# Kernel tuning notes

Hardware: AMD Instinct MI355X
Metric: run time of the kernel (lower is better)

The kernel has to match this reference:

```python
import jax, jax.numpy as jnp
import numpy as np

B, S = 32, 2048
NUM_SKILL = 4096
D = 64   # dim_s
M = 32   # size_m


def setup_inputs() -> dict:
    key = jax.random.key(0)
    ks = jax.random.split(key, 16)
    he = (2.0 / D) ** 0.5  # kaiming-normal-ish scale
    return {
        "question": jax.random.randint(ks[0], (B, S), 0, NUM_SKILL),
        "response": jax.random.randint(ks[1], (B, S), 0, 2),
        "skill": jax.random.randint(ks[2], (B, S), 0, NUM_SKILL),
        "mask": jnp.ones((B, S), jnp.float32),
        "k_c_emb": jax.random.normal(ks[3], (NUM_SKILL, D), jnp.float32) * 0.05,
        "v_c_emb": jax.random.normal(ks[4], (2 * NUM_SKILL, D), jnp.float32) * 0.05,
        "Mk": jax.random.normal(ks[5], (M, D), jnp.float32) * he,
        "Mv0": jax.random.normal(ks[6], (M, D), jnp.float32) * he,
        "e_W": jax.random.normal(ks[7], (D, D), jnp.float32) * he,
        "e_b": jnp.zeros((D,), jnp.float32),
        "a_W": jax.random.normal(ks[8], (D, D), jnp.float32) * he,
        "a_b": jnp.zeros((D,), jnp.float32),
        "f_W": jax.random.normal(ks[9], (2 * D, D), jnp.float32) * (2.0 / (2 * D)) ** 0.5,
        "f_b": jnp.zeros((D,), jnp.float32),
        "p_W": jax.random.normal(ks[10], (D, 1), jnp.float32) * he,
        "p_b": jnp.zeros((1,), jnp.float32),
    }


def reference(question, response, skill, mask, k_c_emb, v_c_emb, Mk, Mv0,
              e_W, e_b, a_W, a_b, f_W, f_b, p_W, p_b):
    num_skill = k_c_emb.shape[0]
    batch = question.shape[0]

    xc = skill + num_skill * response          # [B,S]
    k = k_c_emb[skill]                         # [B,S,D]
    v = v_c_emb[xc]                            # [B,S,D]

    w = jax.nn.softmax(jnp.einsum('bsd,md->bsm', k, Mk), axis=-1)  # [B,S,M]
    e = jax.nn.sigmoid(v @ e_W + e_b)          # [B,S,D]
    a = jnp.tanh(v @ a_W + a_b)                # [B,S,D]

    def step(Mvt, inp):
        wt, et, at, mt = inp                   # [B,M],[B,D],[B,D],[B]
        Mvt_next = Mvt * (1.0 - wt[:, :, None] * et[:, None, :]) \
                   + wt[:, :, None] * at[:, None, :]
        Mvt = jnp.where(mt[:, None, None] == 1, Mvt_next, Mvt)
        return Mvt, Mvt

    xs = (jnp.swapaxes(w, 0, 1), jnp.swapaxes(e, 0, 1),
          jnp.swapaxes(a, 0, 1), jnp.swapaxes(mask, 0, 1))
    Mv_init = jnp.broadcast_to(Mv0[None], (batch, M, D))
    _, Mv_states = jax.lax.scan(step, Mv_init, xs)   # [S,B,M,D]; Mv_states[t] = Mv after t+1 updates

    # Mv[:,1:-1] in torch = states after 1..S-1 updates = Mv_states[0:S-1]
    Mv_used = jnp.swapaxes(Mv_states[:-1], 0, 1)      # [B,S-1,M,D]
    read = jnp.einsum('bsm,bsmd->bsd', w[:, 1:], Mv_used)  # [B,S-1,D]
    f = jnp.tanh(jnp.concatenate([read, k[:, 1:]], axis=-1) @ f_W + f_b)
    # dropout is identity in eval mode
    p = (f @ p_W + p_b).squeeze(-1)                   # [B,S-1]
    return p
```

## Files before the change

kernel.cpp:

```cpp
#include <hip/hip_runtime.h>
#include <hip/hip_bf16.h>
#include <math.h>

#define BB 32
#define SS 2048
#define DD 64
#define MM 32
#define NSKILL 4096
#define CC 64
#define LL 32
#define NOUT (BB * (SS - 1))

__device__ __forceinline__ float sigmoidf_(float x) {
    return 1.f / (1.f + __expf(-x));
}
__device__ __forceinline__ float tanhf_(float x) {
    float t = __expf(-2.f * fabsf(x));
    float r = (1.f - t) / (1.f + t);
    return copysignf(r, x);
}

__global__ __launch_bounds__(256, 2) void k_w(
    const int* __restrict__ skill, const float* __restrict__ k_emb,
    const float* __restrict__ Mk, float* __restrict__ w_out)
{
    __shared__ float kst[64][64];
    const int tid = threadIdx.x;
    const int g = blockIdx.x;
    #pragma unroll
    for (int p = 0; p < 4; ++p) {
        const int r = p * 16 + (tid >> 4);
        const int t = g * 64 + r;
        const float4 kv = ((const float4*)(k_emb + (size_t)skill[t] * DD))[tid & 15];
        *(float4*)&kst[r][(tid & 15) * 4] = kv;
    }
    const int l  = tid & 63;
    const int m  = l & 31;
    const int th = l >> 5;
    const int w  = tid >> 6;
    float4 mk4[16];
    const float4* mkp = (const float4*)(Mk + m * DD);
    #pragma unroll
    for (int q = 0; q < 16; ++q) mk4[q] = mkp[q];
    __syncthreads();

    for (int j = 0; j < 8; ++j) {
        const int tl = w * 16 + j * 2 + th;
        const float4* kp = (const float4*)&kst[tl][0];
        float a0 = 0.f, a1 = 0.f, a2 = 0.f, a3 = 0.f;
        #pragma unroll
        for (int q = 0; q < 16; ++q) {
            const float4 kv = kp[q];
            a0 = fmaf(kv.x, mk4[q].x, a0);
            a1 = fmaf(kv.y, mk4[q].y, a1);
            a2 = fmaf(kv.z, mk4[q].z, a2);
            a3 = fmaf(kv.w, mk4[q].w, a3);
        }
        const float lg = (a0 + a1) + (a2 + a3);
        float mx = lg;
        #pragma unroll
        for (int off = 16; off >= 1; off >>= 1) mx = fmaxf(mx, __shfl_xor(mx, off));
        const float ev = __expf(lg - mx);
        float sm = ev;
        #pragma unroll
        for (int off = 16; off >= 1; off >>= 1) sm += __shfl_xor(sm, off);
        w_out[(size_t)(g * 64 + tl) * MM + m] = ev / sm;
    }
}

__global__ __launch_bounds__(256, 2) void k_ea(
    const int* __restrict__ skill, const int* __restrict__ resp,
    const float* __restrict__ v_emb,
    const float* __restrict__ eW, const float* __restrict__ eb,
    const float* __restrict__ aW, const float* __restrict__ ab,
    float* __restrict__ e_out, float* __restrict__ a_out)
{
    __shared__ float vst[64][64];
    const int tid = threadIdx.x;
    const int g = blockIdx.x;
    #pragma unroll
    for (int p = 0; p < 4; ++p) {
        const int r = p * 16 + (tid >> 4);
        const int t = g * 64 + r;
        const int xc = skill[t] + NSKILL * resp[t];
        const float4 vv = ((const float4*)(v_emb + (size_t)xc * DD))[tid & 15];
        *(float4*)&vst[r][(tid & 15) * 4] = vv;
    }
    const int l = tid & 63;
    const int w = tid >> 6;
    float ew[64], aw[64];
    #pragma unroll
    for (int i = 0; i < 64; ++i) ew[i] = eW[i * DD + l];
    #pragma unroll
    for (int i = 0; i < 64; ++i) aw[i] = aW[i * DD + l];
    const float ebd = eb[l], abd = ab[l];
    __syncthreads();

    for (int j = 0; j < 16; ++j) {
        const int tl = w * 16 + j;
        const float4* vp = (const float4*)&vst[tl][0];
        float e0 = ebd, e1 = 0.f, e2 = 0.f, e3 = 0.f;
        float x0 = abd, x1 = 0.f, x2 = 0.f, x3 = 0.f;
        #pragma unroll
        for (int q = 0; q < 16; ++q) {
            const float4 vv = vp[q];
            e0 = fmaf(vv.x, ew[4*q+0], e0);
            e1 = fmaf(vv.y, ew[4*q+1], e1);
            e2 = fmaf(vv.z, ew[4*q+2], e2);
            e3 = fmaf(vv.w, ew[4*q+3], e3);
            x0 = fmaf(vv.x, aw[4*q+0], x0);
            x1 = fmaf(vv.y, aw[4*q+1], x1);
            x2 = fmaf(vv.z, aw[4*q+2], x2);
            x3 = fmaf(vv.w, aw[4*q+3], x3);
        }
        const size_t t = (size_t)(g * 64 + tl);
        e_out[t * DD + l] = sigmoidf_((e0 + e1) + (e2 + e3));
        a_out[t * DD + l] = tanhf_((x0 + x1) + (x2 + x3));
    }
}

__global__ __launch_bounds__(64, 4) void k_pass1(
    const float* __restrict__ w, const float* __restrict__ mask,
    const float* __restrict__ e, const float* __restrict__ a,
    float* __restrict__ Abar, float* __restrict__ Bbar)
{
    __shared__ float4 wl[LL * 16 / 4];
    const int lane = threadIdx.x;
    const int bc = blockIdx.x >> 1;
    const int mh = blockIdx.x & 1;
    const int b = bc / CC;
    const int c = bc % CC;
    const int t0 = c * LL;

    const float4* wg = (const float4*)(w + (size_t)(b * SS + t0) * MM);
    #pragma unroll
    for (int u = 0; u < 2; ++u) {
        const int q4 = u * 64 + lane;
        const int j = q4 >> 2;
        const int q = q4 & 3;
        const float s = (mask[b * SS + t0 + j] == 1.f) ? 1.f : 0.f;
        float4 wq = wg[j * 8 + mh * 4 + q];
        wq.x *= s; wq.y *= s; wq.z *= s; wq.w *= s;
        wl[q4] = wq;
    }
    __syncthreads();

    float Ab[16], Bb[16];
    #pragma unroll
    for (int i = 0; i < 16; ++i) { Ab[i] = 1.f; Bb[i] = 0.f; }

    const float* ep = e + (size_t)(b * SS + t0) * DD + lane;
    const float* ap = a + (size_t)(b * SS + t0) * DD + lane;
    for (int j = 0; j < LL; ++j) {
        const float ed = ep[j * DD];
        const float ad = ap[j * DD];
        const float4* wlj = wl + j * 4;
        #pragma unroll
        for (int u = 0; u < 4; ++u) {
            const float4 wq = wlj[u];
            float t1;
            t1 = fmaf(-wq.x, ed, 1.f); Ab[4*u+0] *= t1; Bb[4*u+0] = fmaf(Bb[4*u+0], t1, wq.x * ad);
            t1 = fmaf(-wq.y, ed, 1.f); Ab[4*u+1] *= t1; Bb[4*u+1] = fmaf(Bb[4*u+1], t1, wq.y * ad);
            t1 = fmaf(-wq.z, ed, 1.f); Ab[4*u+2] *= t1; Bb[4*u+2] = fmaf(Bb[4*u+2], t1, wq.z * ad);
            t1 = fmaf(-wq.w, ed, 1.f); Ab[4*u+3] *= t1; Bb[4*u+3] = fmaf(Bb[4*u+3], t1, wq.w * ad);
        }
    }
    float* Ao = Abar + (size_t)bc * MM * DD + (size_t)(mh * 16) * DD + lane;
    float* Bo = Bbar + (size_t)bc * MM * DD + (size_t)(mh * 16) * DD + lane;
    #pragma unroll
    for (int i = 0; i < 16; ++i) { Ao[i * DD] = Ab[i]; Bo[i * DD] = Bb[i]; }
}

__global__ __launch_bounds__(256, 2) void k_pass2(
    const float* __restrict__ Abar, float* __restrict__ Bbar_cst,
    const float* __restrict__ Mv0)
{
    const int idx = blockIdx.x * 256 + threadIdx.x;
    const int b = idx >> 11;
    const int md = idx & 2047;
    float s = Mv0[md];
    for (int c = 0; c < CC; ++c) {
        const int off = ((b * CC + c) << 11) + md;
        const float sa = Abar[off];
        const float sb = Bbar_cst[off];
        Bbar_cst[off] = s;
        s = fmaf(s, sa, sb);
    }
}

__global__ __launch_bounds__(64, 4) void k_pass3(
    const float* __restrict__ w, const float* __restrict__ mask,
    const float* __restrict__ e, const float* __restrict__ a,
    const float* __restrict__ cstate, float* __restrict__ readv)
{
    __shared__ float4 wl[LL * MM / 4];
    __shared__ float4 wn[LL * MM / 4];
    const int lane = threadIdx.x;
    const int bc = blockIdx.x >> 1;
    const int dh = blockIdx.x & 1;
    const int b = bc / CC;
    const int c = bc % CC;
    const int t0 = c * LL;
    const bool last = (c == CC - 1);
    const int dof = lane & 31;
    const int mh  = lane >> 5;

    const float4* wg  = (const float4*)(w + (size_t)(b * SS + t0) * MM);
    const float4* wg2 = (const float4*)(w + (size_t)(b * SS + t0 + 1) * MM);
    #pragma unroll
    for (int u = 0; u < 4; ++u) {
        const int q4 = u * 64 + lane;
        const int j = q4 >> 3;
        const float s = (mask[b * SS + t0 + j] == 1.f) ? 1.f : 0.f;
        float4 wq = wg[q4];
        wq.x *= s; wq.y *= s; wq.z *= s; wq.w *= s;
        wl[q4] = wq;
        float4 wq2;
        if (last && q4 >= 248) wq2 = make_float4(0.f, 0.f, 0.f, 0.f);
        else                   wq2 = wg2[q4];
        wn[q4] = wq2;
    }
    __syncthreads();

    float Mv[16];
    const float* cs = cstate + (size_t)bc * MM * DD + (size_t)(mh * 16) * DD
                      + dh * 32 + dof;
    #pragma unroll
    for (int i = 0; i < 16; ++i) Mv[i] = cs[i * DD];

    const float* ep = e + (size_t)(b * SS + t0) * DD + dh * 32 + dof;
    const float* ap = a + (size_t)(b * SS + t0) * DD + dh * 32 + dof;
    float* ro = readv + (size_t)(b * SS + t0 + 1) * DD + dh * 32 + dof;
    for (int j = 0; j < LL; ++j) {
        const float ed = ep[j * DD];
        const float ad = ap[j * DD];
        const float4* wlj = wl + j * 8 + mh * 4;
        const float4* wnj = wn + j * 8 + mh * 4;
        float r0 = 0.f, r1 = 0.f, r2 = 0.f, r3 = 0.f;
        #pragma unroll
        for (int u = 0; u < 4; ++u) {
            const float4 wq = wlj[u];
            const float4 w2 = wnj[u];
            float t1;
            t1 = fmaf(-wq.x, ed, 1.f); Mv[4*u+0] = fmaf(Mv[4*u+0], t1, wq.x * ad); r0 = fmaf(w2.x, Mv[4*u+0], r0);
            t1 = fmaf(-wq.y, ed, 1.f); Mv[4*u+1] = fmaf(Mv[4*u+1], t1, wq.y * ad); r1 = fmaf(w2.y, Mv[4*u+1], r1);
            t1 = fmaf(-wq.z, ed, 1.f); Mv[4*u+2] = fmaf(Mv[4*u+2], t1, wq.z * ad); r2 = fmaf(w2.z, Mv[4*u+2], r2);
            t1 = fmaf(-wq.w, ed, 1.f); Mv[4*u+3] = fmaf(Mv[4*u+3], t1, wq.w * ad); r3 = fmaf(w2.w, Mv[4*u+3], r3);
        }
        float r = (r0 + r1) + (r2 + r3);
        r += __shfl_xor(r, 32);
        if (mh == 0 && !(last && j == LL - 1))
            ro[j * DD] = r;
    }
}

__global__ __launch_bounds__(256, 2) void k_final(
    const float* __restrict__ readv, const int* __restrict__ skill,
    const float* __restrict__ k_emb,
    const float* __restrict__ fW, const float* __restrict__ fb,
    const float* __restrict__ pW, const float* __restrict__ pb,
    float* __restrict__ out)
{
    __shared__ float rst[64][64];
    __shared__ float kst[64][64];
    __shared__ float pbuf[64];
    const int tid = threadIdx.x;
    const int g = blockIdx.x;
    #pragma unroll
    for (int p = 0; p < 4; ++p) {
        const int r = p * 16 + (tid >> 4);
        int o = g * 64 + r;
        if (o >= NOUT) o = 0;
        const int b = o / (SS - 1);
        const int s = o - b * (SS - 1) + 1;
        const size_t tok = (size_t)b * SS + s;
        const int q = tid & 15;
        *(float4*)&rst[r][q * 4] = ((const float4*)(readv + tok * DD))[q];
        *(float4*)&kst[r][q * 4] = ((const float4*)(k_emb + (size_t)skill[tok] * DD))[q];
    }
    const int l = tid & 63;
    const int w = tid >> 6;
    float fw[128];
    #pragma unroll
    for (int i = 0; i < 128; ++i) fw[i] = fW[i * DD + l];
    const float fbd = fb[l], pwd = pW[l];
    __syncthreads();

    for (int j = 0; j < 16; ++j) {
        const int tl = w * 16 + j;
        const float4* rp = (const float4*)&rst[tl][0];
        const float4* kp = (const float4*)&kst[tl][0];
        float f0 = fbd, f1 = 0.f, f2 = 0.f, f3 = 0.f;
        #pragma unroll
        for (int q = 0; q < 16; ++q) {
            const float4 rv = rp[q];
            f0 = fmaf(rv.x, fw[4*q+0], f0);
            f1 = fmaf(rv.y, fw[4*q+1], f1);
            f2 = fmaf(rv.z, fw[4*q+2], f2);
            f3 = fmaf(rv.w, fw[4*q+3], f3);
        }
        #pragma unroll
        for (int q = 0; q < 16; ++q) {
            const float4 kv = kp[q];
            f0 = fmaf(kv.x, fw[64+4*q+0], f0);
            f1 = fmaf(kv.y, fw[64+4*q+1], f1);
            f2 = fmaf(kv.z, fw[64+4*q+2], f2);
            f3 = fmaf(kv.w, fw[64+4*q+3], f3);
        }
        float pv = tanhf_((f0 + f1) + (f2 + f3)) * pwd;
        #pragma unroll
        for (int off = 32; off >= 1; off >>= 1) pv += __shfl_xor(pv, off);
        if (l == 0) pbuf[tl] = pv;
    }
    __syncthreads();
    if (tid < 64) {
        const int o = g * 64 + tid;
        if (o < NOUT) out[o] = pbuf[tid] + pb[0];
    }
}

extern "C" void kernel_launch(void* const* d_in, const int* in_sizes, int n_in,
                              void* d_out, int out_size, void* d_ws, size_t ws_size,
                              hipStream_t stream)
{
    const int*   response = (const int*)d_in[1];
    const int*   skill    = (const int*)d_in[2];
    const float* mask     = (const float*)d_in[3];
    const float* k_emb    = (const float*)d_in[4];
    const float* v_emb    = (const float*)d_in[5];
    const float* Mk       = (const float*)d_in[6];
    const float* Mv0      = (const float*)d_in[7];
    const float* eW       = (const float*)d_in[8];
    const float* ebias    = (const float*)d_in[9];
    const float* aW       = (const float*)d_in[10];
    const float* abias    = (const float*)d_in[11];
    const float* fW       = (const float*)d_in[12];
    const float* fbias    = (const float*)d_in[13];
    const float* pW       = (const float*)d_in[14];
    const float* pbias    = (const float*)d_in[15];
    float* out = (float*)d_out;

    float* ws    = (float*)d_ws;
    float* w_    = ws;
    float* e_    = w_    + (size_t)BB * SS * MM;
    float* a_    = e_    + (size_t)BB * SS * DD;
    float* Abar  = a_    + (size_t)BB * SS * DD;
    float* Bbar  = Abar  + (size_t)BB * CC * MM * DD;
    float* readv = Bbar  + (size_t)BB * CC * MM * DD;

    k_w    <<<1024, 256, 0, stream>>>(skill, k_emb, Mk, w_);
    k_ea   <<<1024, 256, 0, stream>>>(skill, response, v_emb,
                                      eW, ebias, aW, abias, e_, a_);
    k_pass1<<<BB * CC * 2, 64, 0, stream>>>(w_, mask, e_, a_, Abar, Bbar);
    k_pass2<<<256,  256, 0, stream>>>(Abar, Bbar, Mv0);
    k_pass3<<<BB * CC * 2, 64, 0, stream>>>(w_, mask, e_, a_, Bbar, readv);
    k_final<<<1024, 256, 0, stream>>>(readv, skill, k_emb, fW, fbias,
                                      pW, pbias, out);
}
```

Before: 216.1 us.

## Fuse w, e/a projection and chunk-scan pass1 into one front kernel

Merges the softmax-weight kernel, the erase/add projection kernel and the first chunked-scan pass into a single kernel. Each block keeps its 64 timesteps of w, e and a in LDS and computes the per-chunk affine composition directly, so pass1 no longer re-reads those tensors from global memory. Two waves split each 32-step chunk and combine their results through LDS. The pass2 carry loop is also unrolled by four so its loads are issued together. The cost is much higher LDS use per block (about 58 KB), which may limit occupancy, and a less parallel pass1 phase inside the fused kernel.

```diff
diff --git a/kernel.cpp b/kernel.cpp
--- a/kernel.cpp
+++ b/kernel.cpp
@@ -20,144 +20,137 @@
     return copysignf(r, x);
 }
 
-__global__ __launch_bounds__(256, 2) void k_w(
-    const int* __restrict__ skill, const float* __restrict__ k_emb,
-    const float* __restrict__ Mk, float* __restrict__ w_out)
-{
-    __shared__ float kst[64][64];
+__global__ __launch_bounds__(256, 2) void k_front(
+    const int* __restrict__ skill, const int* __restrict__ resp,
+    const float* __restrict__ k_emb, const float* __restrict__ v_emb,
+    const float* __restrict__ Mk,
+    const float* __restrict__ eW, const float* __restrict__ eb,
+    const float* __restrict__ aW, const float* __restrict__ ab,
+    const float* __restrict__ mask,
+    float* __restrict__ w_out, float* __restrict__ e_out, float* __restrict__ a_out,
+    float* __restrict__ Abar, float* __restrict__ Bbar)
+{
+    __shared__ float stage[64 * 64];
+    __shared__ float w_lds[64 * 32];
+    __shared__ float ea_lds[2 * 64 * 64];
+    __shared__ float mk_lds[64];
     const int tid = threadIdx.x;
     const int g = blockIdx.x;
+    const int l = tid & 63;
+    const int wv = tid >> 6;
+
+    if (tid < 64) mk_lds[tid] = mask[g * 64 + tid];
+
     #pragma unroll
     for (int p = 0; p < 4; ++p) {
         const int r = p * 16 + (tid >> 4);
         const int t = g * 64 + r;
         const float4 kv = ((const float4*)(k_emb + (size_t)skill[t] * DD))[tid & 15];
-        *(float4*)&kst[r][(tid & 15) * 4] = kv;
-    }
-    const int l  = tid & 63;
-    const int m  = l & 31;
-    const int th = l >> 5;
-    const int w  = tid >> 6;
-    float4 mk4[16];
-    const float4* mkp = (const float4*)(Mk + m * DD);
-    #pragma unroll
-    for (int q = 0; q < 16; ++q) mk4[q] = mkp[q];
-    __syncthreads();
-
-    for (int j = 0; j < 8; ++j) {
-        const int tl = w * 16 + j * 2 + th;
-        const float4* kp = (const float4*)&kst[tl][0];
-        float a0 = 0.f, a1 = 0.f, a2 = 0.f, a3 = 0.f;
-        #pragma unroll
-        for (int q = 0; q < 16; ++q) {
-            const float4 kv = kp[q];
-            a0 = fmaf(kv.x, mk4[q].x, a0);
-            a1 = fmaf(kv.y, mk4[q].y, a1);
-            a2 = fmaf(kv.z, mk4[q].z, a2);
-            a3 = fmaf(kv.w, mk4[q].w, a3);
-        }
-        const float lg = (a0 + a1) + (a2 + a3);
-        float mx = lg;
-        #pragma unroll
-        for (int off = 16; off >= 1; off >>= 1) mx = fmaxf(mx, __shfl_xor(mx, off));
-        const float ev = __expf(lg - mx);
-        float sm = ev;
-        #pragma unroll
-        for (int off = 16; off >= 1; off >>= 1) sm += __shfl_xor(sm, off);
-        w_out[(size_t)(g * 64 + tl) * MM + m] = ev / sm;
-    }
-}
-
-__global__ __launch_bounds__(256, 2) void k_ea(
-    const int* __restrict__ skill, const int* __restrict__ resp,
-    const float* __restrict__ v_emb,
-    const float* __restrict__ eW, const float* __restrict__ eb,
-    const float* __restrict__ aW, const float* __restrict__ ab,
-    float* __restrict__ e_out, float* __restrict__ a_out)
-{
-    __shared__ float vst[64][64];
-    const int tid = threadIdx.x;
-    const int g = blockIdx.x;
+        *(float4*)&stage[r * 64 + (tid & 15) * 4] = kv;
+    }
+    __syncthreads();
+
+    {
+        const int m  = l & 31;
+        const int th = l >> 5;
+        float4 mk4[16];
+        const float4* mkp = (const float4*)(Mk + m * DD);
+        #pragma unroll
+        for (int q = 0; q < 16; ++q) mk4[q] = mkp[q];
+
+        for (int j = 0; j < 8; ++j) {
+            const int tl = wv * 16 + j * 2 + th;
+            const float4* kp = (const float4*)&stage[tl * 64];
+            float a0 = 0.f, a1 = 0.f, a2 = 0.f, a3 = 0.f;
+            #pragma unroll
+            for (int q = 0; q < 16; ++q) {
+                const float4 kv = kp[q];
+                a0 = fmaf(kv.x, mk4[q].x, a0);
+                a1 = fmaf(kv.y, mk4[q].y, a1);
+                a2 = fmaf(kv.z, mk4[q].z, a2);
+                a3 = fmaf(kv.w, mk4[q].w, a3);
+            }
+            const float lg = (a0 + a1) + (a2 + a3);
+            float mx = lg;
+            #pragma unroll
+            for (int off = 16; off >= 1; off >>= 1) mx = fmaxf(mx, __shfl_xor(mx, off));
+            const float ev = __expf(lg - mx);
+            float sm = ev;
+            #pragma unroll
+            for (int off = 16; off >= 1; off >>= 1) sm += __shfl_xor(sm, off);
+            w_lds[tl * 32 + m] = ev / sm;
+        }
+    }
+    __syncthreads();
+
+    #pragma unroll
+    for (int i = 0; i < 8; ++i) {
+        const int idx = i * 256 + tid;
+        w_out[(size_t)g * 2048 + idx] = w_lds[idx];
+    }
+
     #pragma unroll
     for (int p = 0; p < 4; ++p) {
         const int r = p * 16 + (tid >> 4);
         const int t = g * 64 + r;
         const int xc = skill[t] + NSKILL * resp[t];
         const float4 vv = ((const float4*)(v_emb + (size_t)xc * DD))[tid & 15];
-        *(float4*)&vst[r][(tid & 15) * 4] = vv;
-    }
-    const int l = tid & 63;
-    const int w = tid >> 6;
-    float ew[64], aw[64];
-    #pragma unroll
-    for (int i = 0; i < 64; ++i) ew[i] = eW[i * DD + l];
-    #pragma unroll
-    for (int i = 0; i < 64; ++i) aw[i] = aW[i * DD + l];
-    const float ebd = eb[l], abd = ab[l];
-    __syncthreads();
+        *(float4*)&stage[r * 64 + (tid & 15) * 4] = vv;
+    }
+    __syncthreads();
+
+    {
+        float ew[64], aw[64];
+        #pragma unroll
+        for (int i = 0; i < 64; ++i) ew[i] = eW[i * DD + l];
+        #pragma unroll
+        for (int i = 0; i < 64; ++i) aw[i] = aW[i * DD + l];
+        const float ebd = eb[l], abd = ab[l];
+
+        for (int j = 0; j < 16; ++j) {
+            const int tl = wv * 16 + j;
+            const float4* vp = (const float4*)&stage[tl * 64];
+            float e0 = ebd, e1 = 0.f, e2 = 0.f, e3 = 0.f;
+            float x0 = abd, x1 = 0.f, x2 = 0.f, x3 = 0.f;
+            #pragma unroll
+            for (int q = 0; q < 16; ++q) {
+                const float4 vv = vp[q];
+                e0 = fmaf(vv.x, ew[4*q+0], e0);
+                e1 = fmaf(vv.y, ew[4*q+1], e1);
+                e2 = fmaf(vv.z, ew[4*q+2], e2);
+                e3 = fmaf(vv.w, ew[4*q+3], e3);
+                x0 = fmaf(vv.x, aw[4*q+0], x0);
+                x1 = fmaf(vv.y, aw[4*q+1], x1);
+                x2 = fmaf(vv.z, aw[4*q+2], x2);
+                x3 = fmaf(vv.w, aw[4*q+3], x3);
+            }
+            const float es = sigmoidf_((e0 + e1) + (e2 + e3));
+            const float as = tanhf_((x0 + x1) + (x2 + x3));
+            const size_t t = (size_t)(g * 64 + tl);
+            e_out[t * DD + l] = es;
+            a_out[t * DD + l] = as;
+            ea_lds[tl * 64 + l] = es;
+            ea_lds[4096 + tl * 64 + l] = as;
+        }
+    }
+    __syncthreads();
+
+    const int ch = wv >> 1;
+    const int hf = wv & 1;
+    float Ab[32], Bb[32];
+    #pragma unroll
+    for (int i = 0; i < 32; ++i) { Ab[i] = 1.f; Bb[i] = 0.f; }
 
     for (int j = 0; j < 16; ++j) {
-        const int tl = w * 16 + j;
-        const float4* vp = (const float4*)&vst[tl][0];
-        float e0 = ebd, e1 = 0.f, e2 = 0.f, e3 = 0.f;
-        float x0 = abd, x1 = 0.f, x2 = 0.f, x3 = 0.f;
-        #pragma unroll
-        for (int q = 0; q < 16; ++q) {
-            const float4 vv = vp[q];
-            e0 = fmaf(vv.x, ew[4*q+0], e0);
-            e1 = fmaf(vv.y, ew[4*q+1], e1);
-            e2 = fmaf(vv.z, ew[4*q+2], e2);
-            e3 = fmaf(vv.w, ew[4*q+3], e3);
-            x0 = fmaf(vv.x, aw[4*q+0], x0);
-            x1 = fmaf(vv.y, aw[4*q+1], x1);
-            x2 = fmaf(vv.z, aw[4*q+2], x2);
-            x3 = fmaf(vv.w, aw[4*q+3], x3);
-        }
-        const size_t t = (size_t)(g * 64 + tl);
-        e_out[t * DD + l] = sigmoidf_((e0 + e1) + (e2 + e3));
-        a_out[t * DD + l] = tanhf_((x0 + x1) + (x2 + x3));
-    }
-}
-
-__global__ __launch_bounds__(64, 4) void k_pass1(
-    const float* __restrict__ w, const float* __restrict__ mask,
-    const float* __restrict__ e, const float* __restrict__ a,
-    float* __restrict__ Abar, float* __restrict__ Bbar)
-{
-    __shared__ float4 wl[LL * 16 / 4];
-    const int lane = threadIdx.x;
-    const int bc = blockIdx.x >> 1;
-    const int mh = blockIdx.x & 1;
-    const int b = bc / CC;
-    const int c = bc % CC;
-    const int t0 = c * LL;
-
-    const float4* wg = (const float4*)(w + (size_t)(b * SS + t0) * MM);
-    #pragma unroll
-    for (int u = 0; u < 2; ++u) {
-        const int q4 = u * 64 + lane;
-        const int j = q4 >> 2;
-        const int q = q4 & 3;
-        const float s = (mask[b * SS + t0 + j] == 1.f) ? 1.f : 0.f;
-        float4 wq = wg[j * 8 + mh * 4 + q];
-        wq.x *= s; wq.y *= s; wq.z *= s; wq.w *= s;
-        wl[q4] = wq;
-    }
-    __syncthreads();
-
-    float Ab[16], Bb[16];
-    #pragma unroll
-    for (int i = 0; i < 16; ++i) { Ab[i] = 1.f; Bb[i] = 0.f; }
-
-    const float* ep = e + (size_t)(b * SS + t0) * DD + lane;
-    const float* ap = a + (size_t)(b * SS + t0) * DD + lane;
-    for (int j = 0; j < LL; ++j) {
-        const float ed = ep[j * DD];
-        const float ad = ap[j * DD];
-        const float4* wlj = wl + j * 4;
-        #pragma unroll
-        for (int u = 0; u < 4; ++u) {
-            const float4 wq = wlj[u];
+        const int t = ch * 32 + hf * 16 + j;
+        const float ed = ea_lds[t * 64 + l];
+        const float ad = ea_lds[4096 + t * 64 + l];
+        const float msk = (mk_lds[t] == 1.f) ? 1.f : 0.f;
+        const float4* wr = (const float4*)&w_lds[t * 32];
+        #pragma unroll
+        for (int u = 0; u < 8; ++u) {
+            float4 wq = wr[u];
+            wq.x *= msk; wq.y *= msk; wq.z *= msk; wq.w *= msk;
             float t1;
             t1 = fmaf(-wq.x, ed, 1.f); Ab[4*u+0] *= t1; Bb[4*u+0] = fmaf(Bb[4*u+0], t1, wq.x * ad);
             t1 = fmaf(-wq.y, ed, 1.f); Ab[4*u+1] *= t1; Bb[4*u+1] = fmaf(Bb[4*u+1], t1, wq.y * ad);
@@ -165,10 +158,27 @@
             t1 = fmaf(-wq.w, ed, 1.f); Ab[4*u+3] *= t1; Bb[4*u+3] = fmaf(Bb[4*u+3], t1, wq.w * ad);
         }
     }
-    float* Ao = Abar + (size_t)bc * MM * DD + (size_t)(mh * 16) * DD + lane;
-    float* Bo = Bbar + (size_t)bc * MM * DD + (size_t)(mh * 16) * DD + lane;
-    #pragma unroll
-    for (int i = 0; i < 16; ++i) { Ao[i * DD] = Ab[i]; Bo[i * DD] = Bb[i]; }
+    __syncthreads();
+
+    float* xch = ea_lds;
+    if (hf == 0) {
+        #pragma unroll
+        for (int i = 0; i < 32; ++i) {
+            xch[((ch * 2 + 0) * 32 + i) * 64 + l] = Ab[i];
+            xch[((ch * 2 + 1) * 32 + i) * 64 + l] = Bb[i];
+        }
+    }
+    __syncthreads();
+    if (hf == 1) {
+        const size_t base = ((size_t)g * 2 + ch) * (MM * DD);
+        #pragma unroll
+        for (int i = 0; i < 32; ++i) {
+            const float Aa = xch[((ch * 2 + 0) * 32 + i) * 64 + l];
+            const float Ba = xch[((ch * 2 + 1) * 32 + i) * 64 + l];
+            Abar[base + i * 64 + l] = Aa * Ab[i];
+            Bbar[base + i * 64 + l] = fmaf(Ba, Ab[i], Bb[i]);
+        }
+    }
 }
 
 __global__ __launch_bounds__(256, 2) void k_pass2(
@@ -179,12 +189,20 @@
     const int b = idx >> 11;
     const int md = idx & 2047;
     float s = Mv0[md];
-    for (int c = 0; c < CC; ++c) {
-        const int off = ((b * CC + c) << 11) + md;
-        const float sa = Abar[off];
-        const float sb = Bbar_cst[off];
-        Bbar_cst[off] = s;
-        s = fmaf(s, sa, sb);
+    for (int c = 0; c < CC; c += 4) {
+        const int o0 = ((b * CC + c) << 11) + md;
+        const float sa0 = Abar[o0];
+        const float sb0 = Bbar_cst[o0];
+        const float sa1 = Abar[o0 + 2048];
+        const float sb1 = Bbar_cst[o0 + 2048];
+        const float sa2 = Abar[o0 + 4096];
+        const float sb2 = Bbar_cst[o0 + 4096];
+        const float sa3 = Abar[o0 + 6144];
+        const float sb3 = Bbar_cst[o0 + 6144];
+        Bbar_cst[o0]        = s; s = fmaf(s, sa0, sb0);
+        Bbar_cst[o0 + 2048] = s; s = fmaf(s, sa1, sb1);
+        Bbar_cst[o0 + 4096] = s; s = fmaf(s, sa2, sb2);
+        Bbar_cst[o0 + 6144] = s; s = fmaf(s, sa3, sb3);
     }
 }
 
@@ -348,10 +366,9 @@
     float* Bbar  = Abar  + (size_t)BB * CC * MM * DD;
     float* readv = Bbar  + (size_t)BB * CC * MM * DD;
 
-    k_w    <<<1024, 256, 0, stream>>>(skill, k_emb, Mk, w_);
-    k_ea   <<<1024, 256, 0, stream>>>(skill, response, v_emb,
-                                      eW, ebias, aW, abias, e_, a_);
-    k_pass1<<<BB * CC * 2, 64, 0, stream>>>(w_, mask, e_, a_, Abar, Bbar);
+    k_front<<<1024, 256, 0, stream>>>(skill, response, k_emb, v_emb, Mk,
+                                      eW, ebias, aW, abias, mask,
+                                      w_, e_, a_, Abar, Bbar);
     k_pass2<<<256,  256, 0, stream>>>(Abar, Bbar, Mv0);
     k_pass3<<<BB * CC * 2, 64, 0, stream>>>(w_, mask, e_, a_, Bbar, readv);
     k_final<<<1024, 256, 0, stream>>>(readv, skill, k_emb, fW, fbias,
```

Result: faster. 208.8 us (-3.4%).
